# Performance work log

Hardware: AMD Instinct MI355X
Metric: run time of the kernel (lower is better)

Reference implementation:

```python
import jax, jax.numpy as jnp
import numpy as np

B, N_ATOMS, N_BONDS, HID = 16, 50000, 100000, 128


def _lin(x, w, b):
    # torch nn.Linear: y = x @ W^T + b
    return x @ w.T + b


def setup_inputs() -> dict:
    key = jax.random.key(0)
    ks = jax.random.split(key, 16)

    def w(k, shape, fan_in):
        return jax.random.normal(k, shape, jnp.float32) * (1.0 / np.sqrt(fan_in))

    return {
        "alpha": jax.random.normal(ks[0], (B, 1), jnp.float32),
        "baseline_positions": jax.random.normal(ks[1], (B, N_ATOMS, 3), jnp.float32),
        "bonds": jax.random.randint(ks[2], (N_BONDS, 2), 0, N_ATOMS, jnp.int32),
        # standard branch: Linear(1,256) -> ResBlock(256) x2 -> Linear(256, n_atoms*3)
        "w_in": w(ks[3], (256, 1), 1), "b_in": jnp.zeros((256,), jnp.float32),
        "rb1_w1": w(ks[4], (256, 256), 256), "rb1_b1": jnp.zeros((256,), jnp.float32),
        "rb1_w2": w(ks[5], (256, 256), 256), "rb1_b2": jnp.zeros((256,), jnp.float32),
        "rb2_w1": w(ks[6], (256, 256), 256), "rb2_b1": jnp.zeros((256,), jnp.float32),
        "rb2_w2": w(ks[7], (256, 256), 256), "rb2_b2": jnp.zeros((256,), jnp.float32),
        "w_out": w(ks[8], (N_ATOMS * 3, 256), 256), "b_out": jnp.zeros((N_ATOMS * 3,), jnp.float32),
        # graph branch
        "msg_w": w(ks[9], (HID, 3), 3), "msg_b": jnp.zeros((HID,), jnp.float32),
        "upd_w": w(ks[10], (3, HID), HID), "upd_b": jnp.zeros((3,), jnp.float32),
        "go_w": w(ks[11], (3, 3), 3), "go_b": jnp.zeros((3,), jnp.float32),
    }


def reference(alpha, baseline_positions, bonds,
              w_in, b_in,
              rb1_w1, rb1_b1, rb1_w2, rb1_b2,
              rb2_w1, rb2_b1, rb2_w2, rb2_b2,
              w_out, b_out,
              msg_w, msg_b, upd_w, upd_b, go_w, go_b):
    b, n_atoms, _ = baseline_positions.shape

    # ---- standard branch (Dropout is identity in eval mode) ----
    x = jax.nn.relu(_lin(alpha, w_in, b_in))
    x = jax.nn.relu(_lin(jax.nn.relu(_lin(x, rb1_w1, rb1_b1)), rb1_w2, rb1_b2) + x)
    x = jax.nn.relu(_lin(jax.nn.relu(_lin(x, rb2_w1, rb2_b1)), rb2_w2, rb2_b2) + x)
    standard_out = _lin(x, w_out, b_out).reshape(b, n_atoms, 3)

    # ---- graph branch: symmetric edge list, mean aggregation ----
    src = jnp.concatenate([bonds[:, 0], bonds[:, 1]])  # [2E]
    dst = jnp.concatenate([bonds[:, 1], bonds[:, 0]])  # [2E]
    deg = jnp.zeros((n_atoms,), jnp.float32).at[dst].add(1.0)
    safe_deg = jnp.maximum(deg, 1.0)[None, :, None]
    has_nb = (deg > 0)[None, :, None]

    h = baseline_positions
    for _ in range(2):  # n_iters
        # mean of linear(neighbor feats) == linear(mean of neighbor feats) (affine)
        nb_sum = jnp.zeros((b, n_atoms, 3), h.dtype).at[:, dst, :].add(h[:, src, :])
        nb_mean = nb_sum / safe_deg
        msgs = jnp.where(has_nb, _lin(nb_mean, msg_w, msg_b), 0.0)  # [B,N,128]
        h = h + _lin(msgs, upd_w, upd_b)

    graph_out = _lin(h, go_w, go_b)
    return standard_out + graph_out
```

## Files before the change

kernel.cpp:

```cpp
#include <hip/hip_runtime.h>

#define N_ATOMS 50000
#define N_BONDS 100000
#define BATCH   16
#define N3      150000
#define BK      32

#define X_OFF    0
#define MC_OFF   4096
#define CNT_OFF  4112
#define BKT_OFF  54112
#define HA_OFF   1654112
#define HB_OFF   4054112
#define WS_FAST_BYTES ((size_t)(HB_OFF + 2400000) * 4)

#define DEGF_OFF 4112
#define HT_OFF   54144
#define NB_OFF   2454144

typedef __bf16 bf16x8 __attribute__((ext_vector_type(8)));
typedef float  f32x4  __attribute__((ext_vector_type(4)));


__device__ __forceinline__ void mlp_block(int b, int j,
    const float* __restrict__ alpha,
    const float* __restrict__ w_in, const float* __restrict__ b_in,
    const float* __restrict__ w1a, const float* __restrict__ b1a,
    const float* __restrict__ w1b, const float* __restrict__ b1b,
    const float* __restrict__ w2a, const float* __restrict__ b2a,
    const float* __restrict__ w2b, const float* __restrict__ b2b,
    float* xs, float* ts, float* __restrict__ x_out)
{
    float v = fmaxf(w_in[j] * alpha[b] + b_in[j], 0.f);
    xs[j] = v;
    __syncthreads();

    float acc = b1a[j];
    const float4* wr = reinterpret_cast<const float4*>(w1a + j * 256);
    #pragma unroll 8
    for (int k4 = 0; k4 < 64; ++k4) {
        float4 w = wr[k4];
        acc += w.x * xs[4*k4] + w.y * xs[4*k4+1] + w.z * xs[4*k4+2] + w.w * xs[4*k4+3];
    }
    ts[j] = fmaxf(acc, 0.f);
    __syncthreads();

    acc = b1b[j] + xs[j];
    wr = reinterpret_cast<const float4*>(w1b + j * 256);
    #pragma unroll 8
    for (int k4 = 0; k4 < 64; ++k4) {
        float4 w = wr[k4];
        acc += w.x * ts[4*k4] + w.y * ts[4*k4+1] + w.z * ts[4*k4+2] + w.w * ts[4*k4+3];
    }
    v = fmaxf(acc, 0.f);
    __syncthreads();
    xs[j] = v;
    __syncthreads();

    acc = b2a[j];
    wr = reinterpret_cast<const float4*>(w2a + j * 256);
    #pragma unroll 8
    for (int k4 = 0; k4 < 64; ++k4) {
        float4 w = wr[k4];
        acc += w.x * xs[4*k4] + w.y * xs[4*k4+1] + w.z * xs[4*k4+2] + w.w * xs[4*k4+3];
    }
    ts[j] = fmaxf(acc, 0.f);
    __syncthreads();

    acc = b2b[j] + xs[j];
    wr = reinterpret_cast<const float4*>(w2b + j * 256);
    #pragma unroll 8
    for (int k4 = 0; k4 < 64; ++k4) {
        float4 w = wr[k4];
        acc += w.x * ts[4*k4] + w.y * ts[4*k4+1] + w.z * ts[4*k4+2] + w.w * ts[4*k4+3];
    }
    x_out[b * 256 + j] = fmaxf(acc, 0.f);
}

struct PrepParams {
    const float *alpha, *pos;
    const float *w_in, *b_in, *w1a, *b1a, *w1b, *b1b, *w2a, *b2a, *w2b, *b2b;
    const float *msg_w, *msg_b, *upd_w, *upd_b;
    float *x, *mc;
    int *cnt;
    float *hA;
};

__global__ __launch_bounds__(256) void prep_kernel(PrepParams p)
{
    __shared__ float smem[512];
    const int bid = blockIdx.x, tid = threadIdx.x;
    const int nb = gridDim.x;

    if (bid < 16) {
        mlp_block(bid, tid, p.alpha, p.w_in, p.b_in,
                  p.w1a, p.b1a, p.w1b, p.b1b, p.w2a, p.b2a, p.w2b, p.b2b,
                  smem, smem + 256, p.x);
    } else if (bid == 16) {
        if (tid < 9) {
            int d = tid / 3, dp = tid % 3;
            float s = 0.f;
            for (int k = 0; k < 128; ++k) s += p.upd_w[d*128 + k] * p.msg_w[k*3 + dp];
            p.mc[tid] = s;
        } else if (tid < 12) {
            int d = tid - 9;
            float s = p.upd_b[d];
            for (int k = 0; k < 128; ++k) s += p.upd_w[d*128 + k] * p.msg_b[k];
            p.mc[9 + d] = s;
        }
    } else {
        const int i0 = (bid - 17) * 256 + tid;
        const int st = (nb - 17) * 256;
        if (i0 < N_ATOMS / 4)
            ((int4*)p.cnt)[i0] = make_int4(0, 0, 0, 0);
        for (int i = i0; i < N_ATOMS * 48; i += st) {
            int n = i / 48, c = i - n * 48;
            int b = c / 3, d = c - b * 3;
            p.hA[i] = p.pos[(b * N_ATOMS + n) * 3 + d];
        }
    }
}

__global__ void fill_kernel(const int* __restrict__ bonds, int* __restrict__ cnt,
                            int* __restrict__ bucket)
{
    int e = blockIdx.x * blockDim.x + threadIdx.x;
    if (e >= N_BONDS) return;
    int a = bonds[2*e], b = bonds[2*e + 1];
    int sa = atomicAdd(cnt + a, 1);
    if (sa < BK) bucket[a * BK + sa] = b;
    int sb = atomicAdd(cnt + b, 1);
    if (sb < BK) bucket[b * BK + sb] = a;
}

__global__ void gather_kernel(const int* __restrict__ cnt, const int* __restrict__ bucket,
                              const float* __restrict__ mc, const float* __restrict__ upd_b,
                              const float* __restrict__ h_in, float* __restrict__ h_out)
{
    int t = blockIdx.x * blockDim.x + threadIdx.x;
    if (t >= N_ATOMS * BATCH) return;
    int n = t >> 4, b = t & 15;
    int dg = cnt[n];
    int base = n * 48 + b * 3;
    float d0, d1, d2;
    if (dg > 0) {
        int m = dg > BK ? BK : dg;
        float s0 = 0.f, s1 = 0.f, s2 = 0.f;
        const int* bk = bucket + n * BK;
        for (int j = 0; j < m; ++j) {
            const float* hs = h_in + bk[j] * 48 + b * 3;
            s0 += hs[0]; s1 += hs[1]; s2 += hs[2];
        }
        float inv = 1.f / (float)dg;
        s0 *= inv; s1 *= inv; s2 *= inv;
        d0 = mc[9]  + mc[0]*s0 + mc[1]*s1 + mc[2]*s2;
        d1 = mc[10] + mc[3]*s0 + mc[4]*s1 + mc[5]*s2;
        d2 = mc[11] + mc[6]*s0 + mc[7]*s1 + mc[8]*s2;
    } else {
        d0 = upd_b[0]; d1 = upd_b[1]; d2 = upd_b[2];
    }
    h_out[base]     = h_in[base]     + d0;
    h_out[base + 1] = h_in[base + 1] + d1;
    h_out[base + 2] = h_in[base + 2] + d2;
}

__global__ __launch_bounds__(256) void out_kernel(
    const float* __restrict__ w_out, const float* __restrict__ b_out,
    const float* __restrict__ x, const float* __restrict__ h_t,
    const float* __restrict__ go_w, const float* __restrict__ go_b,
    float* __restrict__ out)
{
    const int lane = threadIdx.x & 63;
    const int widx = threadIdx.x >> 6;
    const int wave = blockIdx.x * 4 + widx;
    const int g  = lane >> 4;
    const int mn = lane & 15;

    bf16x8 afrag[8];
    const float* xrow = x + mn * 256 + g * 8;
    #pragma unroll
    for (int kb = 0; kb < 8; ++kb) {
        float4 lo = *reinterpret_cast<const float4*>(xrow + kb * 32);
        float4 hi = *reinterpret_cast<const float4*>(xrow + kb * 32 + 4);
        bf16x8 a;
        a[0] = (__bf16)lo.x; a[1] = (__bf16)lo.y; a[2] = (__bf16)lo.z; a[3] = (__bf16)lo.w;
        a[4] = (__bf16)hi.x; a[5] = (__bf16)hi.y; a[6] = (__bf16)hi.z; a[7] = (__bf16)hi.w;
        afrag[kb] = a;
    }

    #pragma unroll 1
    for (int t = 0; t < 4; ++t) {
        const int tile = wave * 4 + t;
        if (tile >= 9375) break;
        const int r = tile * 16 + mn;
        const float* wrow = w_out + (size_t)r * 256 + g * 8;

        f32x4 acc = {0.f, 0.f, 0.f, 0.f};
        #pragma unroll
        for (int kb = 0; kb < 8; ++kb) {
            float4 lo = *reinterpret_cast<const float4*>(wrow + kb * 32);
            float4 hi = *reinterpret_cast<const float4*>(wrow + kb * 32 + 4);
            bf16x8 bfr;
            bfr[0] = (__bf16)lo.x; bfr[1] = (__bf16)lo.y; bfr[2] = (__bf16)lo.z; bfr[3] = (__bf16)lo.w;
            bfr[4] = (__bf16)hi.x; bfr[5] = (__bf16)hi.y; bfr[6] = (__bf16)hi.z; bfr[7] = (__bf16)hi.w;
            acc = __builtin_amdgcn_mfma_f32_16x16x32_bf16(afrag[kb], bfr, acc, 0, 0, 0);
        }

        const int n = r / 3, d = r - 3 * n;
        const float g0 = go_w[d*3], g1 = go_w[d*3 + 1], g2 = go_w[d*3 + 2];
        const float gb = go_b[d] + b_out[r];
        #pragma unroll
        for (int j = 0; j < 4; ++j) {
            const int b = g * 4 + j;
            const float* hb = h_t + n * 48 + b * 3;
            float gaff = gb + g0 * hb[0] + g1 * hb[1] + g2 * hb[2];
            out[(size_t)b * N3 + r] = acc[j] + gaff;
        }
    }
}

__global__ void zero4_kernel(int4* __restrict__ p, int n4)
{
    int t = blockIdx.x * 256 + threadIdx.x;
    if (t < n4) p[t] = make_int4(0, 0, 0, 0);
}

__global__ void mlp_head_kernel(const float* __restrict__ alpha,
    const float* __restrict__ w_in, const float* __restrict__ b_in,
    const float* __restrict__ w1a, const float* __restrict__ b1a,
    const float* __restrict__ w1b, const float* __restrict__ b1b,
    const float* __restrict__ w2a, const float* __restrict__ b2a,
    const float* __restrict__ w2b, const float* __restrict__ b2b,
    const float* __restrict__ msg_w, const float* __restrict__ msg_b,
    const float* __restrict__ upd_w, const float* __restrict__ upd_b,
    float* __restrict__ x_out, float* __restrict__ mc)
{
    const int b = blockIdx.x, j = threadIdx.x;
    if (b == 16) {
        if (j < 9) {
            int d = j / 3, dp = j % 3;
            float s = 0.f;
            for (int k = 0; k < 128; ++k) s += upd_w[d*128 + k] * msg_w[k*3 + dp];
            mc[j] = s;
        } else if (j < 12) {
            int d = j - 9;
            float s = upd_b[d];
            for (int k = 0; k < 128; ++k) s += upd_w[d*128 + k] * msg_b[k];
            mc[9 + d] = s;
        }
        return;
    }
    __shared__ float xs[256];
    __shared__ float ts[256];
    mlp_block(b, j, alpha, w_in, b_in, w1a, b1a, w1b, b1b, w2a, b2a, w2b, b2b,
              xs, ts, x_out);
}

__global__ void transpose_in_kernel(const float* __restrict__ pos, float* __restrict__ h_t)
{
    int t = blockIdx.x * blockDim.x + threadIdx.x;
    if (t >= N_ATOMS * 48) return;
    int n = t / 48, c = t % 48;
    int b = c / 3, d = c % 3;
    h_t[t] = pos[(b * N_ATOMS + n) * 3 + d];
}

__global__ void degf_kernel(const int* __restrict__ bonds, float* __restrict__ deg)
{
    int e = blockIdx.x * blockDim.x + threadIdx.x;
    if (e >= N_BONDS) return;
    atomicAdd(deg + bonds[2*e],     1.f);
    atomicAdd(deg + bonds[2*e + 1], 1.f);
}

__global__ void scatter_kernel(const int* __restrict__ bonds,
                               const float* __restrict__ h_t, float* __restrict__ nb_t)
{
    int t = blockIdx.x * 192 + threadIdx.x;
    int e = t / 48, c = t % 48;
    if (e >= N_BONDS) return;
    int a  = bonds[2*e];
    int bb = bonds[2*e + 1];
    float va = h_t[a  * 48 + c];
    float vb = h_t[bb * 48 + c];
    atomicAdd(nb_t + bb * 48 + c, va);
    atomicAdd(nb_t + a  * 48 + c, vb);
}

__global__ void update_kernel(const float* __restrict__ nb_t, const float* __restrict__ deg,
                              const float* __restrict__ mc, const float* __restrict__ upd_b,
                              float* __restrict__ h_t)
{
    int t = blockIdx.x * blockDim.x + threadIdx.x;
    if (t >= N_ATOMS * BATCH) return;
    int n = t >> 4;
    int base = n * 48 + (t & 15) * 3;
    float dg = deg[n];
    float d0, d1, d2;
    if (dg > 0.f) {
        float inv = 1.f / dg;
        float m0 = nb_t[base] * inv, m1 = nb_t[base+1] * inv, m2 = nb_t[base+2] * inv;
        d0 = mc[9]  + mc[0]*m0 + mc[1]*m1 + mc[2]*m2;
        d1 = mc[10] + mc[3]*m0 + mc[4]*m1 + mc[5]*m2;
        d2 = mc[11] + mc[6]*m0 + mc[7]*m1 + mc[8]*m2;
    } else {
        d0 = upd_b[0]; d1 = upd_b[1]; d2 = upd_b[2];
    }
    h_t[base]     += d0;
    h_t[base + 1] += d1;
    h_t[base + 2] += d2;
}

extern "C" void kernel_launch(void* const* d_in, const int* in_sizes, int n_in,
                              void* d_out, int out_size, void* d_ws, size_t ws_size,
                              hipStream_t stream)
{
    const float* alpha = (const float*)d_in[0];
    const float* pos   = (const float*)d_in[1];
    const int*   bonds = (const int*)  d_in[2];
    const float* w_in  = (const float*)d_in[3];
    const float* b_in  = (const float*)d_in[4];
    const float* w1a   = (const float*)d_in[5];
    const float* b1a   = (const float*)d_in[6];
    const float* w1b   = (const float*)d_in[7];
    const float* b1b   = (const float*)d_in[8];
    const float* w2a   = (const float*)d_in[9];
    const float* b2a   = (const float*)d_in[10];
    const float* w2b   = (const float*)d_in[11];
    const float* b2b   = (const float*)d_in[12];
    const float* w_out = (const float*)d_in[13];
    const float* b_out = (const float*)d_in[14];
    const float* msg_w = (const float*)d_in[15];
    const float* msg_b = (const float*)d_in[16];
    const float* upd_w = (const float*)d_in[17];
    const float* upd_b = (const float*)d_in[18];
    const float* go_w  = (const float*)d_in[19];
    const float* go_b  = (const float*)d_in[20];

    float* out = (float*)d_out;
    float* ws  = (float*)d_ws;
    float* x   = ws + X_OFF;
    float* mc  = ws + MC_OFF;

    float* h_final;
    if (ws_size >= WS_FAST_BYTES) {
        PrepParams pp;
        pp.alpha = alpha; pp.pos = pos;
        pp.w_in = w_in; pp.b_in = b_in;
        pp.w1a = w1a; pp.b1a = b1a; pp.w1b = w1b; pp.b1b = b1b;
        pp.w2a = w2a; pp.b2a = b2a; pp.w2b = w2b; pp.b2b = b2b;
        pp.msg_w = msg_w; pp.msg_b = msg_b; pp.upd_w = upd_w; pp.upd_b = upd_b;
        pp.x = x; pp.mc = mc;
        pp.cnt = (int*)(ws + CNT_OFF);
        pp.hA  = ws + HA_OFF;
        prep_kernel<<<1024, 256, 0, stream>>>(pp);

        int* cnt    = (int*)(ws + CNT_OFF);
        int* bucket = (int*)(ws + BKT_OFF);
        float* hA   = ws + HA_OFF;
        float* hB   = ws + HB_OFF;

        fill_kernel<<<(N_BONDS + 255) / 256, 256, 0, stream>>>(bonds, cnt, bucket);
        gather_kernel<<<(N_ATOMS * BATCH + 255) / 256, 256, 0, stream>>>(cnt, bucket, mc, upd_b, hA, hB);
        gather_kernel<<<(N_ATOMS * BATCH + 255) / 256, 256, 0, stream>>>(cnt, bucket, mc, upd_b, hB, hA);
        h_final = hA;
    } else {
        float* degf = ws + DEGF_OFF;
        float* h_t  = ws + HT_OFF;
        size_t need_full = (size_t)(NB_OFF + N_ATOMS * 48) * sizeof(float);
        float* nb_t = (ws_size >= need_full) ? (ws + NB_OFF) : out;

        mlp_head_kernel<<<17, 256, 0, stream>>>(alpha, w_in, b_in,
                                                w1a, b1a, w1b, b1b,
                                                w2a, b2a, w2b, b2b,
                                                msg_w, msg_b, upd_w, upd_b, x, mc);
        zero4_kernel<<<(N_ATOMS / 4 + 255) / 256, 256, 0, stream>>>((int4*)degf, N_ATOMS / 4);
        degf_kernel<<<(N_BONDS + 255) / 256, 256, 0, stream>>>(bonds, degf);
        transpose_in_kernel<<<(N_ATOMS * 48 + 255) / 256, 256, 0, stream>>>(pos, h_t);
        for (int it = 0; it < 2; ++it) {
            zero4_kernel<<<(N_ATOMS * 48 / 4 + 255) / 256, 256, 0, stream>>>((int4*)nb_t, N_ATOMS * 48 / 4);
            scatter_kernel<<<25000, 192, 0, stream>>>(bonds, h_t, nb_t);
            update_kernel<<<(N_ATOMS * BATCH + 255) / 256, 256, 0, stream>>>(nb_t, degf, mc, upd_b, h_t);
        }
        h_final = h_t;
    }

    out_kernel<<<586, 256, 0, stream>>>(w_out, b_out, x, h_final, go_w, go_b, out);
}
```

Before: 116.6 us.

## Double-buffer w_out tiles into LDS via async global_load_lds in out_kernel

```diff
diff --git a/kernel.cpp b/kernel.cpp
--- a/kernel.cpp
+++ b/kernel.cpp
@@ -5,6 +5,7 @@
 #define BATCH   16
 #define N3      150000
 #define BK      32
+#define NTILES  9375
 
 #define X_OFF    0
 #define MC_OFF   4096
@@ -164,15 +165,14 @@
     h_out[base + 2] = h_in[base + 2] + d2;
 }
 
-__global__ __launch_bounds__(256) void out_kernel(
+__global__ __launch_bounds__(64) void out_kernel(
     const float* __restrict__ w_out, const float* __restrict__ b_out,
     const float* __restrict__ x, const float* __restrict__ h_t,
     const float* __restrict__ go_w, const float* __restrict__ go_b,
     float* __restrict__ out)
 {
-    const int lane = threadIdx.x & 63;
-    const int widx = threadIdx.x >> 6;
-    const int wave = blockIdx.x * 4 + widx;
+    __shared__ float lds[2][16][268];
+    const int lane = threadIdx.x;
     const int g  = lane >> 4;
     const int mn = lane & 15;
 
@@ -188,24 +188,47 @@
         afrag[kb] = a;
     }
 
+    const int t0 = blockIdx.x * 4;
+
+    auto stage16 = [&](int tile, int buf) {
+        const float* gsrc = w_out + (size_t)tile * 16 * 256;
+        #pragma unroll
+        for (int i = 0; i < 16; ++i) {
+            __builtin_amdgcn_global_load_lds(
+                (const __attribute__((address_space(1))) unsigned int*)(gsrc + i * 256 + lane * 4),
+                (__attribute__((address_space(3))) unsigned int*)(&lds[buf][i][0]),
+                16, 0, 0);
+        }
+    };
+
+    if (t0 < NTILES) stage16(t0, 0);
+
     #pragma unroll 1
     for (int t = 0; t < 4; ++t) {
-        const int tile = wave * 4 + t;
-        if (tile >= 9375) break;
-        const int r = tile * 16 + mn;
-        const float* wrow = w_out + (size_t)r * 256 + g * 8;
-
+        const int tile = t0 + t;
+        if (tile >= NTILES) break;
+        const bool nxt = (t + 1 < 4) && (tile + 1 < NTILES);
+        if (nxt) {
+            stage16(tile + 1, (t + 1) & 1);
+            asm volatile("s_waitcnt vmcnt(16)" ::: "memory");
+        } else {
+            asm volatile("s_waitcnt vmcnt(0)" ::: "memory");
+        }
+        __builtin_amdgcn_sched_barrier(0);
+
+        const float* lrow = &lds[t & 1][mn][0];
         f32x4 acc = {0.f, 0.f, 0.f, 0.f};
         #pragma unroll
         for (int kb = 0; kb < 8; ++kb) {
-            float4 lo = *reinterpret_cast<const float4*>(wrow + kb * 32);
-            float4 hi = *reinterpret_cast<const float4*>(wrow + kb * 32 + 4);
+            float4 lo = *reinterpret_cast<const float4*>(lrow + kb * 32 + g * 8);
+            float4 hi = *reinterpret_cast<const float4*>(lrow + kb * 32 + g * 8 + 4);
             bf16x8 bfr;
             bfr[0] = (__bf16)lo.x; bfr[1] = (__bf16)lo.y; bfr[2] = (__bf16)lo.z; bfr[3] = (__bf16)lo.w;
             bfr[4] = (__bf16)hi.x; bfr[5] = (__bf16)hi.y; bfr[6] = (__bf16)hi.z; bfr[7] = (__bf16)hi.w;
             acc = __builtin_amdgcn_mfma_f32_16x16x32_bf16(afrag[kb], bfr, acc, 0, 0, 0);
         }
 
+        const int r = tile * 16 + mn;
         const int n = r / 3, d = r - 3 * n;
         const float g0 = go_w[d*3], g1 = go_w[d*3 + 1], g2 = go_w[d*3 + 2];
         const float gb = go_b[d] + b_out[r];
@@ -385,5 +408,5 @@
         h_final = h_t;
     }
 
-    out_kernel<<<586, 256, 0, stream>>>(w_out, b_out, x, h_final, go_w, go_b, out);
-}
+    out_kernel<<<2344, 64, 0, stream>>>(w_out, b_out, x, h_final, go_w, go_b, out);
+}
```

Result: faster. 112.8 us, median of 2 (-3.2%).
